# Performance work log

Hardware: AMD Instinct MI355X
Metric: run time of the kernel (lower is better)

The kernel has to match this reference:

```python
import math
import jax, jax.numpy as jnp
import numpy as np

B, S, D, H = 2, 2048, 1024, 16
DH = D // H


def setup_inputs() -> dict:
    key = jax.random.key(0)
    ks = jax.random.split(key, 12)
    s = 1.0 / math.sqrt(D)
    return {
        "x_q": jax.random.normal(ks[0], (B, S, D), jnp.float32),
        "x_k": jax.random.normal(ks[1], (B, S, D), jnp.float32),
        "x_v": jax.random.normal(ks[2], (B, S, D), jnp.float32),
        "mask": jax.random.randint(ks[3], (B, S), 0, 2) > 0,
        "Wq": jax.random.normal(ks[4], (D, D), jnp.float32) * s,
        "bq": jnp.zeros((D,), jnp.float32),
        "Wk": jax.random.normal(ks[5], (D, D), jnp.float32) * s,
        "bk": jnp.zeros((D,), jnp.float32),
        "Wv": jax.random.normal(ks[6], (D, D), jnp.float32) * s,
        "bv": jnp.zeros((D,), jnp.float32),
        "Wo": jax.random.normal(ks[7], (D, D), jnp.float32) * s,
        "bo": jnp.zeros((D,), jnp.float32),
    }


def reference(x_q, x_k, x_v, mask, Wq, bq, Wk, bk, Wv, bv, Wo, bo):
    # nn.Linear: y = x @ W^T + b
    Q = jnp.einsum('bsd,ed->bse', x_q, Wq) + bq
    K = jnp.einsum('bsd,ed->bse', x_k, Wk) + bk
    V = jnp.einsum('bsd,ed->bse', x_v, Wv) + bv
    b, sq, d = Q.shape
    # split(dim_split, 2) + cat(dim=0) == per-head attention on [B,S,H,DH]
    Qh = Q.reshape(b, sq, H, DH)
    Kh = K.reshape(b, -1, H, DH)
    Vh = V.reshape(b, -1, H, DH)
    scores = jnp.einsum('bqhd,bkhd->bhqk', Qh, Kh) / math.sqrt(DH)
    # inf_mask: -1e9 where mask is False, broadcast over heads and queries
    scores = scores + jnp.where(mask[:, None, None, :], 0.0, -1e9)
    A = jax.nn.softmax(scores, axis=-1)  # dropout is identity in eval
    out = jnp.einsum('bhqk,bkhd->bqhd', A, Vh).reshape(b, sq, d)
    return jnp.einsum('bsd,ed->bse', out, Wo) + bo
```

## Files before the change

kernel.cpp:

```cpp
#include <hip/hip_runtime.h>
#include <hip/hip_bf16.h>
#include <stdint.h>

#define BB  2
#define SS  2048
#define DDIM 1024
#define HH  16
#define DH  64

typedef __attribute__((ext_vector_type(8))) short short8;
typedef __attribute__((ext_vector_type(4))) short short4v;
typedef __attribute__((ext_vector_type(4))) float float4v;

#define AS1 __attribute__((address_space(1)))
#define AS3 __attribute__((address_space(3)))

static __device__ __forceinline__ void gl2lds16(const void* g, void* l) {
  __builtin_amdgcn_global_load_lds((const AS1 unsigned int*)g,
                                   (AS3 unsigned int*)l, 16, 0, 0);
}

static __device__ __forceinline__ float bf2f(short s) {
  union { unsigned u; float f; } c;
  c.u = ((unsigned)(unsigned short)s) << 16;
  return c.f;
}
static __device__ __forceinline__ short f2bf(float f) {
  union { float ff; unsigned u; } c;
  c.ff = f;
  unsigned u = c.u;
  u += 0x7fffu + ((u >> 16) & 1u);
  return (short)(u >> 16);
}

static __device__ __forceinline__ unsigned cvtpk(float x, float y) {
  union { __hip_bfloat162 h; unsigned u; } c;
  c.h = __float22bfloat162_rn(float2{x, y});
  return c.u;
}

#if __has_builtin(__builtin_amdgcn_exp2f)
static __device__ __forceinline__ float exp2fast(float x) { return __builtin_amdgcn_exp2f(x); }
#else
static __device__ __forceinline__ float exp2fast(float x) { return __expf(x * 0.69314718056f); }
#endif

static __device__ __forceinline__ int detect_f32(const void* p) {
  const float* f = (const float*)p;
  int ok = 1;
#pragma unroll
  for (int i = 0; i < 16; i++) {
    float a = fabsf(f[i]);
    ok &= (a > 1e-10f && a < 1e4f) ? 1 : 0;
  }
  return ok;
}

struct CvtArgs {
  const void* xq; const void* xk; const void* xv;
  const void* wq; const void* wk; const void* wv; const void* wo;
  const void* b0; const void* b1; const void* b2; const void* b3;
  const int* mask;
  short* dst;
  float* mw;
};

__global__ __launch_bounds__(256)
void cvt_kernel(CvtArgs a) {
  const int f32m = detect_f32(a.xq);
  const size_t gtid = (size_t)blockIdx.x * blockDim.x + threadIdx.x;
  const size_t stride = (size_t)gridDim.x * blockDim.x;
  const size_t M4 = (size_t)4 << 20, M1 = (size_t)1 << 20, TOT = (size_t)16 << 20;
  for (size_t i = gtid; i * 4 < TOT; i += stride) {
    const size_t idx = i * 4;
    const void* src;
    size_t off;
    if (idx < 3 * M4) {
      size_t xi = idx / M4;
      off = idx & (M4 - 1);
      src = (xi == 0) ? a.xq : (xi == 1) ? a.xk : a.xv;
    } else {
      size_t wi = (idx - 3 * M4) / M1;
      off = idx & (M1 - 1);
      src = (wi == 0) ? a.wq : (wi == 1) ? a.wk : (wi == 2) ? a.wv : a.wo;
    }
    short4v o;
    if (f32m) {
      float4v v = *(const float4v*)((const float*)src + off);
      union { unsigned u[2]; short4v s; } pk;
      pk.u[0] = cvtpk(v[0], v[1]);
      pk.u[1] = cvtpk(v[2], v[3]);
      o = pk.s;
    } else {
      o = *(const short4v*)((const short*)src + off);
    }
    *(short4v*)(a.dst + idx) = o;
  }
  if (gtid < 1024) {
    const void* bs[4] = {a.b0, a.b1, a.b2, a.b3};
#pragma unroll
    for (int j = 0; j < 4; j++) {
      short v = f32m ? f2bf(((const float*)bs[j])[gtid])
                     : ((const short*)bs[j])[gtid];
      a.dst[TOT + (size_t)j * 1024 + gtid] = v;
    }
  }
  if (gtid < BB * SS)
    a.mw[gtid] = a.mask[gtid] ? -23.083120654223414f : -1e9f;
}

struct GemmArgs {
  const short* x[3];
  const short* w[3];
  const short* b[3];
  short* o[3];
  const void* probe;
  int tmask;
  int detect_out;
};

template <int MW>
__global__ __launch_bounds__(256)
void gemm_kernel(GemmArgs a) {
  constexpr int GK = 1024, GN = 1024;
  __shared__ alignas(16) short As[32 * MW * 32];
  __shared__ alignas(16) short Bs[128 * 32];

  const int t = threadIdx.x;
  const int w = t >> 6, l = t & 63, l15 = l & 15, qd = l >> 4;
  const int bn = blockIdx.x, bm = blockIdx.y, mat = blockIdx.z;

  const short* X  = a.x[mat];
  const short* W  = a.w[mat];
  const short* Bi = a.b[mat];
  short* O        = a.o[mat];
  const int transposed = (a.tmask >> mat) & 1;

  const short* Ag = X + (size_t)bm * (32 * MW) * GK;
  const short* Bg = W + (size_t)bn * 128 * GK;

  const int L0 = t, L1 = 256 + t;
  const int r0 = L0 >> 2, g0 = (L0 & 3) ^ ((r0 >> 1) & 3);
  const int r1 = L1 >> 2, g1 = (L1 & 3) ^ ((r1 >> 1) & 3);
  const size_t off0 = (size_t)r0 * GK + g0 * 8;
  const size_t off1 = (size_t)r1 * GK + g1 * 8;

  float4v acc[MW][4];
#pragma unroll
  for (int i = 0; i < MW; i++)
#pragma unroll
    for (int j = 0; j < 4; j++) acc[i][j] = (float4v){0.f, 0.f, 0.f, 0.f};

  const int wm = (w >> 1) * 16 * MW, wn = (w & 1) * 64;

  for (int k0 = 0; k0 < GK; k0 += 32) {
    gl2lds16(Ag + off0 + k0, (char*)As + L0 * 16);
    if (MW == 4) gl2lds16(Ag + off1 + k0, (char*)As + L1 * 16);
    gl2lds16(Bg + off0 + k0, (char*)Bs + L0 * 16);
    gl2lds16(Bg + off1 + k0, (char*)Bs + L1 * 16);
    __syncthreads();

    short8 af[MW], bf[4];
#pragma unroll
    for (int i = 0; i < MW; i++) {
      int m = wm + i * 16 + l15;
      af[i] = *(const short8*)((const char*)As + (m * 4 + (qd ^ ((m >> 1) & 3))) * 16);
    }
#pragma unroll
    for (int j = 0; j < 4; j++) {
      int n = wn + j * 16 + l15;
      bf[j] = *(const short8*)((const char*)Bs + (n * 4 + (qd ^ ((n >> 1) & 3))) * 16);
    }
#pragma unroll
    for (int i = 0; i < MW; i++)
#pragma unroll
      for (int j = 0; j < 4; j++)
        acc[i][j] = __builtin_amdgcn_mfma_f32_16x16x32_bf16(af[i], bf[j], acc[i][j], 0, 0, 0);
    __syncthreads();
  }

  if (!transposed) {
    const int outf32 = a.detect_out ? detect_f32(a.probe) : 0;
    float bj[4];
#pragma unroll
    for (int j = 0; j < 4; j++) bj[j] = bf2f(Bi[bn * 128 + wn + j * 16 + l15]);
#pragma unroll
    for (int i = 0; i < MW; i++) {
      int mgl = bm * (32 * MW) + wm + i * 16 + qd * 4;
#pragma unroll
      for (int j = 0; j < 4; j++) {
        int ngl = bn * 128 + wn + j * 16 + l15;
        if (outf32) {
          float* Of = (float*)O;
#pragma unroll
          for (int r = 0; r < 4; r++)
            Of[(size_t)(mgl + r) * GN + ngl] = acc[i][j][r] + bj[j];
        } else {
#pragma unroll
          for (int r = 0; r < 4; r++)
            O[(size_t)(mgl + r) * GN + ngl] = f2bf(acc[i][j][r] + bj[j]);
        }
      }
    }
  } else {
#pragma unroll
    for (int j = 0; j < 4; j++) {
      int ngl = bn * 128 + wn + j * 16 + l15;
      float bb = bf2f(Bi[ngl]);
#pragma unroll
      for (int i = 0; i < MW; i++) {
        int mgl = bm * (32 * MW) + wm + i * 16 + qd * 4;
        int bidx = mgl >> 11;
        int s = mgl & (SS - 1);
        short4v v;
#pragma unroll
        for (int r = 0; r < 4; r++) v[r] = f2bf(acc[i][j][r] + bb);
        *(short4v*)(O + (size_t)bidx * DDIM * SS + (size_t)ngl * SS + s) = v;
      }
    }
  }
}

__global__ __launch_bounds__(256)
void flash_kernel(const short* __restrict__ Q, const short* __restrict__ K,
                  const short* __restrict__ Vt, const float* __restrict__ Mw,
                  short* __restrict__ At) {
  __shared__ alignas(16) short Ks[2][64 * 64];
  __shared__ alignas(16) short Vs[2][64 * 64];
  __shared__ alignas(16) float madd[2][64];

  const int t = threadIdx.x;
  const int w = t >> 6, l = t & 63, l15 = l & 15, qd = l >> 4;
  const int bh = blockIdx.x, qt = blockIdx.y;
  const int b = bh >> 4, h = bh & 15;
  const int q0 = qt * 128 + w * 32;

  const float SC = 0.125f * 1.44269504f;

  short8 qf[2][2];
#pragma unroll
  for (int g = 0; g < 2; g++) {
    const short* Qb = Q + ((size_t)(b * SS + q0 + 16 * g + l15)) * DDIM + h * 64;
#pragma unroll
    for (int c = 0; c < 2; c++) qf[g][c] = *(const short8*)(Qb + 32 * c + 8 * qd);
  }

  const short ov = (l15 == 0) ? (short)0x3F80 : (short)0;
  const short8 onesf = {ov, ov, ov, ov, ov, ov, ov, ov};

  const int kr = t >> 3;
  const int pkr = ((kr & 12) << 1) | ((kr & 16) >> 2) | (kr & 3);
  const short* Kg = K + ((size_t)(b * SS + pkr)) * DDIM + h * 64
                    + ((t & 7) ^ (kr & 7)) * 8;
  const int vr = t >> 3;
  const short* Vg = Vt + (size_t)b * DDIM * SS + (size_t)(h * 64 + vr) * SS
                    + ((t & 7) ^ (vr & 7)) * 8;
  const float* MwB = Mw + b * SS;

  float4v oacc[2][4], oaccl[2];
#pragma unroll
  for (int g = 0; g < 2; g++) {
    oaccl[g] = (float4v){0.f, 0.f, 0.f, 0.f};
#pragma unroll
    for (int mt = 0; mt < 4; mt++) oacc[g][mt] = (float4v){0.f, 0.f, 0.f, 0.f};
  }

  const int swz = l15 & 7;

  gl2lds16(Kg, (char*)Ks[0] + t * 16);
  gl2lds16(Kg + (size_t)32 * DDIM, (char*)Ks[0] + 4096 + t * 16);
  gl2lds16(Vg, (char*)Vs[0] + t * 16);
  gl2lds16(Vg + 32 * SS, (char*)Vs[0] + 4096 + t * 16);
  float mwN = 0.f;
  if (t < 64) {
    madd[0][t] = MwB[t];
    mwN = MwB[64 + t];
  }

  for (int i = 0; i < 32; i++) {
    const int cur = i & 1, nxt = cur ^ 1;
    asm volatile("s_waitcnt vmcnt(0) lgkmcnt(0)\n\ts_barrier" ::: "memory");

    if (i < 31) {
      const size_t ko = (size_t)((i + 1) * 64) * DDIM;
      gl2lds16(Kg + ko, (char*)Ks[nxt] + t * 16);
      gl2lds16(Kg + ko + (size_t)32 * DDIM, (char*)Ks[nxt] + 4096 + t * 16);
      const int vo = (i + 1) * 64;
      gl2lds16(Vg + vo, (char*)Vs[nxt] + t * 16);
      gl2lds16(Vg + vo + 32 * SS, (char*)Vs[nxt] + 4096 + t * 16);
    }
    if (t < 64) {
      madd[nxt][t] = mwN;
      int idx = (i + 2) * 64 + t;
      if (idx > SS - 1) idx = SS - 1;
      mwN = MwB[idx];
    }

    const short* ksb = Ks[cur];
    const short* vsb = Vs[cur];

    float4v sacc[2][4];
#pragma unroll
    for (int g = 0; g < 2; g++)
#pragma unroll
      for (int mt = 0; mt < 4; mt++) sacc[g][mt] = (float4v){0.f, 0.f, 0.f, 0.f};
#pragma unroll
    for (int mt = 0; mt < 4; mt++) {
#pragma unroll
      for (int c = 0; c < 2; c++) {
        short8 kf = *(const short8*)(ksb + (mt * 16 + l15) * 64 + (((4 * c + qd) ^ swz) * 8));
#pragma unroll
        for (int g = 0; g < 2; g++)
          sacc[g][mt] = __builtin_amdgcn_mfma_f32_16x16x32_bf16(kf, qf[g][c], sacc[g][mt], 0, 0, 0);
      }
    }

#pragma unroll
    for (int pp = 0; pp < 2; pp++) {
      float4v ma0 = *(const float4v*)(&madd[cur][32 * pp + 8 * qd]);
      float4v ma1 = *(const float4v*)(&madd[cur][32 * pp + 8 * qd + 4]);
      short8 vf[4];
#pragma unroll
      for (int mt = 0; mt < 4; mt++)
        vf[mt] = *(const short8*)(vsb + (mt * 16 + l15) * 64 + (((4 * pp + qd) ^ swz) * 8));
#pragma unroll
      for (int g = 0; g < 2; g++) {
        float p0[4], p1[4];
#pragma unroll
        for (int r = 0; r < 4; r++) {
          p0[r] = exp2fast(fmaf(sacc[g][2 * pp][r],     SC, ma0[r]));
          p1[r] = exp2fast(fmaf(sacc[g][2 * pp + 1][r], SC, ma1[r]));
        }
        union { unsigned u[4]; short8 v8; } pk;
        pk.u[0] = cvtpk(p0[0], p0[1]);
        pk.u[1] = cvtpk(p0[2], p0[3]);
        pk.u[2] = cvtpk(p1[0], p1[1]);
        pk.u[3] = cvtpk(p1[2], p1[3]);
#pragma unroll
        for (int mt = 0; mt < 4; mt++)
          oacc[g][mt] = __builtin_amdgcn_mfma_f32_16x16x32_bf16(vf[mt], pk.v8, oacc[g][mt], 0, 0, 0);
        oaccl[g] = __builtin_amdgcn_mfma_f32_16x16x32_bf16(onesf, pk.v8, oaccl[g], 0, 0, 0);
      }
    }
  }

#pragma unroll
  for (int g = 0; g < 2; g++) {
    const float lg = __shfl(oaccl[g][0], l15);
    const float inv = 1.f / lg;
    short* Og = At + ((size_t)(b * SS + q0 + 16 * g + l15)) * DDIM + h * 64;
#pragma unroll
    for (int mt = 0; mt < 4; mt++) {
      short4v v;
#pragma unroll
      for (int r = 0; r < 4; r++) v[r] = f2bf(oacc[g][mt][r] * inv);
      *(short4v*)(Og + mt * 16 + qd * 4) = v;
    }
  }
}

extern "C" void kernel_launch(void* const* d_in, const int* in_sizes, int n_in,
                              void* d_out, int out_size, void* d_ws, size_t ws_size,
                              hipStream_t stream) {
  (void)in_sizes; (void)n_in; (void)out_size; (void)ws_size;
  const int* mask = (const int*)d_in[3];

  char* ws = (char*)d_ws;
  short* wsBF = (short*)ws;
  const size_t M1 = (size_t)1 << 20;
  short* Qb = (short*)(ws + (size_t)34 * M1);
  short* Kb = (short*)(ws + (size_t)42 * M1);
  short* Vt = (short*)(ws + (size_t)50 * M1);
  short* At = (short*)(ws + (size_t)58 * M1);
  float* Mw = (float*)(ws + (size_t)66 * M1);

  CvtArgs c;
  c.xq = d_in[0]; c.xk = d_in[1]; c.xv = d_in[2];
  c.wq = d_in[4]; c.wk = d_in[6]; c.wv = d_in[8]; c.wo = d_in[10];
  c.b0 = d_in[5]; c.b1 = d_in[7]; c.b2 = d_in[9]; c.b3 = d_in[11];
  c.mask = mask; c.dst = wsBF; c.mw = Mw;
  hipLaunchKernelGGL(cvt_kernel, dim3(4096), dim3(256), 0, stream, c);

  GemmArgs a1;
  a1.x[0] = wsBF;            a1.x[1] = wsBF + 4 * M1;  a1.x[2] = wsBF + 8 * M1;
  a1.w[0] = wsBF + 12 * M1;  a1.w[1] = wsBF + 13 * M1; a1.w[2] = wsBF + 14 * M1;
  a1.b[0] = wsBF + 16 * M1;  a1.b[1] = wsBF + 16 * M1 + 1024;
  a1.b[2] = wsBF + 16 * M1 + 2048;
  a1.o[0] = Qb; a1.o[1] = Kb; a1.o[2] = Vt;
  a1.probe = d_in[0];
  a1.tmask = 4;
  a1.detect_out = 0;
  hipLaunchKernelGGL(HIP_KERNEL_NAME(gemm_kernel<4>), dim3(8, 32, 3), dim3(256),
                     0, stream, a1);

  hipLaunchKernelGGL(flash_kernel, dim3(32, 16), dim3(256), 0, stream,
                     Qb, Kb, Vt, Mw, At);

  GemmArgs a2;
  a2.x[0] = At;             a2.w[0] = wsBF + 15 * M1;
  a2.b[0] = wsBF + 16 * M1 + 3072;
  a2.o[0] = (short*)d_out;
  a2.x[1] = a2.x[2] = At; a2.w[1] = a2.w[2] = a2.w[0];
  a2.b[1] = a2.b[2] = a2.b[0]; a2.o[1] = a2.o[2] = a2.o[0];
  a2.probe = d_in[0];
  a2.tmask = 0;
  a2.detect_out = 1;
  hipLaunchKernelGGL(HIP_KERNEL_NAME(gemm_kernel<2>), dim3(8, 64, 1), dim3(256),
                     0, stream, a2);
}
```

Before: 239.7 us.

## Shrink flash blocks to two waves and read mask directly from global

The flash attention kernel now uses 128-thread blocks covering 64 queries, launched as a 1D grid of 1024 blocks ordered so the 32 batch-heads of one query tile are adjacent. Each thread issues four global-to-LDS loads per K/V tile instead of two, and the LDS mask staging is replaced by direct vector loads of the mask from global memory each iteration. The lgkmcnt wait is dropped from the barrier. The aim is more blocks for better CU occupancy and less LDS traffic, at the cost of each K/V tile being loaded by twice as many blocks.

```diff
diff --git a/kernel.cpp b/kernel.cpp
--- a/kernel.cpp
+++ b/kernel.cpp
@@ -221,19 +221,19 @@
   }
 }
 
-__global__ __launch_bounds__(256)
+__global__ __launch_bounds__(128)
 void flash_kernel(const short* __restrict__ Q, const short* __restrict__ K,
                   const short* __restrict__ Vt, const float* __restrict__ Mw,
                   short* __restrict__ At) {
   __shared__ alignas(16) short Ks[2][64 * 64];
   __shared__ alignas(16) short Vs[2][64 * 64];
-  __shared__ alignas(16) float madd[2][64];
 
   const int t = threadIdx.x;
   const int w = t >> 6, l = t & 63, l15 = l & 15, qd = l >> 4;
-  const int bh = blockIdx.x, qt = blockIdx.y;
+  const int x = blockIdx.x;
+  const int bh = x & 31, qt = x >> 5;
   const int b = bh >> 4, h = bh & 15;
-  const int q0 = qt * 128 + w * 32;
+  const int q0 = qt * 64 + w * 32;
 
   const float SC = 0.125f * 1.44269504f;
 
@@ -249,12 +249,13 @@
   const short8 onesf = {ov, ov, ov, ov, ov, ov, ov, ov};
 
   const int kr = t >> 3;
-  const int pkr = ((kr & 12) << 1) | ((kr & 16) >> 2) | (kr & 3);
-  const short* Kg = K + ((size_t)(b * SS + pkr)) * DDIM + h * 64
-                    + ((t & 7) ^ (kr & 7)) * 8;
-  const int vr = t >> 3;
-  const short* Vg = Vt + (size_t)b * DDIM * SS + (size_t)(h * 64 + vr) * SS
-                    + ((t & 7) ^ (vr & 7)) * 8;
+  const int kc = (t & 7) ^ (kr & 7);
+  int pk[4];
+#pragma unroll
+  for (int c = 0; c < 4; c++)
+    pk[c] = ((c >> 1) << 5) | ((kr >> 2) << 3) | ((c & 1) << 2) | (kr & 3);
+  const short* KgB = K + (size_t)(b * SS) * DDIM + h * 64 + kc * 8;
+  const short* VgB = Vt + (size_t)b * DDIM * SS + (size_t)(h * 64 + kr) * SS + kc * 8;
   const float* MwB = Mw + b * SS;
 
   float4v oacc[2][4], oaccl[2];
@@ -267,34 +268,34 @@
 
   const int swz = l15 & 7;
 
-  gl2lds16(Kg, (char*)Ks[0] + t * 16);
-  gl2lds16(Kg + (size_t)32 * DDIM, (char*)Ks[0] + 4096 + t * 16);
-  gl2lds16(Vg, (char*)Vs[0] + t * 16);
-  gl2lds16(Vg + 32 * SS, (char*)Vs[0] + 4096 + t * 16);
-  float mwN = 0.f;
-  if (t < 64) {
-    madd[0][t] = MwB[t];
-    mwN = MwB[64 + t];
-  }
+#pragma unroll
+  for (int c = 0; c < 4; c++)
+    gl2lds16(KgB + (size_t)pk[c] * DDIM, (char*)Ks[0] + c * 2048 + t * 16);
+#pragma unroll
+  for (int c = 0; c < 4; c++)
+    gl2lds16(VgB + (size_t)(16 * c) * SS, (char*)Vs[0] + c * 2048 + t * 16);
 
   for (int i = 0; i < 32; i++) {
     const int cur = i & 1, nxt = cur ^ 1;
-    asm volatile("s_waitcnt vmcnt(0) lgkmcnt(0)\n\ts_barrier" ::: "memory");
+    asm volatile("s_waitcnt vmcnt(0)\n\ts_barrier" ::: "memory");
 
     if (i < 31) {
       const size_t ko = (size_t)((i + 1) * 64) * DDIM;
-      gl2lds16(Kg + ko, (char*)Ks[nxt] + t * 16);
-      gl2lds16(Kg + ko + (size_t)32 * DDIM, (char*)Ks[nxt] + 4096 + t * 16);
       const int vo = (i + 1) * 64;
-      gl2lds16(Vg + vo, (char*)Vs[nxt] + t * 16);
-      gl2lds16(Vg + vo + 32 * SS, (char*)Vs[nxt] + 4096 + t * 16);
-    }
-    if (t < 64) {
-      madd[nxt][t] = mwN;
-      int idx = (i + 2) * 64 + t;
-      if (idx > SS - 1) idx = SS - 1;
-      mwN = MwB[idx];
-    }
+#pragma unroll
+      for (int c = 0; c < 4; c++)
+        gl2lds16(KgB + ko + (size_t)pk[c] * DDIM, (char*)Ks[nxt] + c * 2048 + t * 16);
+#pragma unroll
+      for (int c = 0; c < 4; c++)
+        gl2lds16(VgB + vo + (size_t)(16 * c) * SS, (char*)Vs[nxt] + c * 2048 + t * 16);
+    }
+
+    float4v ma[2][2];
+#pragma unroll
+    for (int pp = 0; pp < 2; pp++)
+#pragma unroll
+      for (int s = 0; s < 2; s++)
+        ma[pp][s] = *(const float4v*)(MwB + i * 64 + 32 * pp + 8 * qd + 4 * s);
 
     const short* ksb = Ks[cur];
     const short* vsb = Vs[cur];
@@ -317,8 +318,6 @@
 
 #pragma unroll
     for (int pp = 0; pp < 2; pp++) {
-      float4v ma0 = *(const float4v*)(&madd[cur][32 * pp + 8 * qd]);
-      float4v ma1 = *(const float4v*)(&madd[cur][32 * pp + 8 * qd + 4]);
       short8 vf[4];
 #pragma unroll
       for (int mt = 0; mt < 4; mt++)
@@ -328,18 +327,18 @@
         float p0[4], p1[4];
 #pragma unroll
         for (int r = 0; r < 4; r++) {
-          p0[r] = exp2fast(fmaf(sacc[g][2 * pp][r],     SC, ma0[r]));
-          p1[r] = exp2fast(fmaf(sacc[g][2 * pp + 1][r], SC, ma1[r]));
+          p0[r] = exp2fast(fmaf(sacc[g][2 * pp][r],     SC, ma[pp][0][r]));
+          p1[r] = exp2fast(fmaf(sacc[g][2 * pp + 1][r], SC, ma[pp][1][r]));
         }
-        union { unsigned u[4]; short8 v8; } pk;
-        pk.u[0] = cvtpk(p0[0], p0[1]);
-        pk.u[1] = cvtpk(p0[2], p0[3]);
-        pk.u[2] = cvtpk(p1[0], p1[1]);
-        pk.u[3] = cvtpk(p1[2], p1[3]);
+        union { unsigned u[4]; short8 v8; } pkk;
+        pkk.u[0] = cvtpk(p0[0], p0[1]);
+        pkk.u[1] = cvtpk(p0[2], p0[3]);
+        pkk.u[2] = cvtpk(p1[0], p1[1]);
+        pkk.u[3] = cvtpk(p1[2], p1[3]);
 #pragma unroll
         for (int mt = 0; mt < 4; mt++)
-          oacc[g][mt] = __builtin_amdgcn_mfma_f32_16x16x32_bf16(vf[mt], pk.v8, oacc[g][mt], 0, 0, 0);
-        oaccl[g] = __builtin_amdgcn_mfma_f32_16x16x32_bf16(onesf, pk.v8, oaccl[g], 0, 0, 0);
+          oacc[g][mt] = __builtin_amdgcn_mfma_f32_16x16x32_bf16(vf[mt], pkk.v8, oacc[g][mt], 0, 0, 0);
+        oaccl[g] = __builtin_amdgcn_mfma_f32_16x16x32_bf16(onesf, pkk.v8, oaccl[g], 0, 0, 0);
       }
     }
   }
@@ -393,7 +392,7 @@
   hipLaunchKernelGGL(HIP_KERNEL_NAME(gemm_kernel<4>), dim3(8, 32, 3), dim3(256),
                      0, stream, a1);
 
-  hipLaunchKernelGGL(flash_kernel, dim3(32, 16), dim3(256), 0, stream,
+  hipLaunchKernelGGL(flash_kernel, dim3(1024), dim3(128), 0, stream,
                      Qb, Kb, Vt, Mw, At);
 
   GemmArgs a2;
```

Measured after the change: 249.8 us. +4.2%, slower.

## Double GEMM K-tile to 64 and remap blocks for L2 locality

Applied to the files above, without the earlier changes.

The projection GEMM now stages a 64-wide K slice per iteration instead of 32. This halves the number of barrier pairs and loop iterations, and the LDS swizzle changes to an 8-chunk XOR pattern. Block indices are also remapped so that neighbouring workgroups share A and B tiles, which should improve cache reuse. The cost is double the shared memory per block, which may lower occupancy. The remap also hardcodes an 8-wide grid assumption.

```diff
diff --git a/kernel.cpp b/kernel.cpp
--- a/kernel.cpp
+++ b/kernel.cpp
@@ -123,12 +123,17 @@
 __global__ __launch_bounds__(256)
 void gemm_kernel(GemmArgs a) {
   constexpr int GK = 1024, GN = 1024;
-  __shared__ alignas(16) short As[32 * MW * 32];
-  __shared__ alignas(16) short Bs[128 * 32];
+  __shared__ alignas(16) short As[32 * MW * 64];
+  __shared__ alignas(16) short Bs[128 * 64];
 
   const int t = threadIdx.x;
   const int w = t >> 6, l = t & 63, l15 = l & 15, qd = l >> 4;
-  const int bn = blockIdx.x, bm = blockIdx.y, mat = blockIdx.z;
+  const int mat = blockIdx.z;
+
+  const int p = blockIdx.x + 8 * blockIdx.y;
+  const int r_ = p & 7, q_ = p >> 3;
+  const int bn = (r_ & 3) * 2 + (q_ & 1);
+  const int bm = (r_ >> 2) * (64 / MW) + (q_ >> 1);
 
   const short* X  = a.x[mat];
   const short* W  = a.w[mat];
@@ -139,11 +144,8 @@
   const short* Ag = X + (size_t)bm * (32 * MW) * GK;
   const short* Bg = W + (size_t)bn * 128 * GK;
 
-  const int L0 = t, L1 = 256 + t;
-  const int r0 = L0 >> 2, g0 = (L0 & 3) ^ ((r0 >> 1) & 3);
-  const int r1 = L1 >> 2, g1 = (L1 & 3) ^ ((r1 >> 1) & 3);
-  const size_t off0 = (size_t)r0 * GK + g0 * 8;
-  const size_t off1 = (size_t)r1 * GK + g1 * 8;
+  const int sr = t >> 3, sc = t & 7;
+  const int schk = (sc ^ (sr & 7)) * 8;
 
   float4v acc[MW][4];
 #pragma unroll
@@ -152,30 +154,40 @@
     for (int j = 0; j < 4; j++) acc[i][j] = (float4v){0.f, 0.f, 0.f, 0.f};
 
   const int wm = (w >> 1) * 16 * MW, wn = (w & 1) * 64;
-
-  for (int k0 = 0; k0 < GK; k0 += 32) {
-    gl2lds16(Ag + off0 + k0, (char*)As + L0 * 16);
-    if (MW == 4) gl2lds16(Ag + off1 + k0, (char*)As + L1 * 16);
-    gl2lds16(Bg + off0 + k0, (char*)Bs + L0 * 16);
-    gl2lds16(Bg + off1 + k0, (char*)Bs + L1 * 16);
+  const int swz = l15 & 7;
+
+  for (int k0 = 0; k0 < GK; k0 += 64) {
+#pragma unroll
+    for (int c = 0; c < MW; c++) {
+      int rr = 32 * c + sr;
+      gl2lds16(Ag + (size_t)rr * GK + k0 + schk, (char*)As + (rr * 8 + sc) * 16);
+    }
+#pragma unroll
+    for (int c = 0; c < 4; c++) {
+      int rr = 32 * c + sr;
+      gl2lds16(Bg + (size_t)rr * GK + k0 + schk, (char*)Bs + (rr * 8 + sc) * 16);
+    }
     __syncthreads();
 
-    short8 af[MW], bf[4];
-#pragma unroll
-    for (int i = 0; i < MW; i++) {
-      int m = wm + i * 16 + l15;
-      af[i] = *(const short8*)((const char*)As + (m * 4 + (qd ^ ((m >> 1) & 3))) * 16);
-    }
-#pragma unroll
-    for (int j = 0; j < 4; j++) {
-      int n = wn + j * 16 + l15;
-      bf[j] = *(const short8*)((const char*)Bs + (n * 4 + (qd ^ ((n >> 1) & 3))) * 16);
-    }
-#pragma unroll
-    for (int i = 0; i < MW; i++)
-#pragma unroll
-      for (int j = 0; j < 4; j++)
-        acc[i][j] = __builtin_amdgcn_mfma_f32_16x16x32_bf16(af[i], bf[j], acc[i][j], 0, 0, 0);
+#pragma unroll
+    for (int ks = 0; ks < 2; ks++) {
+      short8 af[MW], bf[4];
+#pragma unroll
+      for (int i = 0; i < MW; i++) {
+        int m = wm + i * 16 + l15;
+        af[i] = *(const short8*)((const char*)As + (m * 8 + ((ks * 4 + qd) ^ swz)) * 16);
+      }
+#pragma unroll
+      for (int j = 0; j < 4; j++) {
+        int n = wn + j * 16 + l15;
+        bf[j] = *(const short8*)((const char*)Bs + (n * 8 + ((ks * 4 + qd) ^ swz)) * 16);
+      }
+#pragma unroll
+      for (int i = 0; i < MW; i++)
+#pragma unroll
+        for (int j = 0; j < 4; j++)
+          acc[i][j] = __builtin_amdgcn_mfma_f32_16x16x32_bf16(af[i], bf[j], acc[i][j], 0, 0, 0);
+    }
     __syncthreads();
   }
 
```

Measured after the change: 230.9 us. -3.7%, faster.
